# Performance work log

Hardware: AMD Instinct MI355X
Metric: run time of the kernel (lower is better)

The kernel has to match this reference:

```python
import jax, jax.numpy as jnp
import numpy as np

E, K, MULT = 8, 2, 4          # num_experts, top_k, ffn mult
CF = 1.25                     # capacity_factor


def setup_inputs() -> dict:
    key = jax.random.key(0)
    ks = jax.random.split(key, 8)
    B, T, C = 4, 2048, 1024
    H = C * MULT
    s = 0.02
    return {
        "x": jax.random.normal(ks[0], (B, T, C), jnp.float32),
        "rw": jax.random.normal(ks[1], (E, C), jnp.float32) * s,   # router weight [E,C]
        "rb": jnp.zeros((E,), jnp.float32),                        # router bias
        "w1": jax.random.normal(ks[2], (E, C, H), jnp.float32) * s,
        "b1": jnp.zeros((E, H), jnp.float32),
        "w2": jax.random.normal(ks[3], (E, H, C), jnp.float32) * s,
        "b2": jnp.zeros((E, C), jnp.float32),
    }


def reference(x, rw, rb, w1, b1, w2, b2):
    B, T, C = x.shape
    N = B * T
    cap = int(CF * N / E)                      # static capacity per expert
    xf = x.reshape(N, C)
    logits = xf @ rw.T + rb                    # [N,E]
    probs = jax.nn.softmax(logits, axis=-1)
    topk_probs, topk_idx = jax.lax.top_k(probs, K)      # [N,K]
    topk_probs = topk_probs / topk_probs.sum(-1, keepdims=True)

    # Flatten (token, choice) row-major == torch.where(mask) ordering
    flat_idx = topk_idx.reshape(-1)            # [N*K] expert id per slot
    flat_gate = topk_probs.reshape(-1)         # [N*K]
    onehot = jax.nn.one_hot(flat_idx, E, dtype=jnp.int32)          # [N*K,E]
    pos = (jnp.cumsum(onehot, axis=0) - 1)[jnp.arange(N * K), flat_idx]  # rank within expert
    keep = pos < cap                           # first-come-first-served capacity drop
    tok = jnp.arange(N * K) // K               # owning token of each slot

    # Dispatch into [E, cap] buffers; dropped slots go to a dump slot at the end
    buf = jnp.where(keep, flat_idx * cap + pos, E * cap)
    gate_buf = jnp.zeros(E * cap + 1, x.dtype).at[buf].add(flat_gate)[:E * cap]
    tok_buf = jnp.zeros(E * cap + 1, jnp.int32).at[buf].set(tok)[:E * cap]

    inp = xf[tok_buf].reshape(E, cap, C)       # gathered expert inputs
    h = jax.nn.gelu(jnp.einsum('eic,ech->eih', inp, w1) + b1[:, None, :], approximate=False)
    out = jnp.einsum('eih,ehc->eic', h, w2) + b2[:, None, :]
    out = out * gate_buf.reshape(E, cap, 1)    # empty slots have gate 0 -> zero contribution

    y = jnp.zeros((N, C), x.dtype).at[tok_buf].add(out.reshape(E * cap, C))

    # Aux load-balancing loss
    imp = probs.sum(0)
    imp = imp / imp.sum()
    load = jnp.minimum(onehot.sum(0).astype(x.dtype), cap)   # kept token counts
    load = load / load.sum()
    aux_loss = (imp * load).sum() * (E ** 2)
    return y.reshape(B, T, C), aux_loss
```

## Files before the change

kernel.cpp:

```cpp
#include <hip/hip_runtime.h>
#include <hip/hip_bf16.h>
#include <math.h>

#define NE    8
#define KTOP  2
#define CDIM  1024
#define HDIM  4096
#define NTOK  8192
#define CAPE  1280
#define NSLOT (NTOK * KTOP)
#define G1BLK 640

typedef __bf16 bf16x8 __attribute__((ext_vector_type(8)));
typedef __bf16 bf16x4 __attribute__((ext_vector_type(4)));
typedef float  f32x4  __attribute__((ext_vector_type(4)));

#define GAS __attribute__((address_space(1)))
#define LAS __attribute__((address_space(3)))

__device__ __forceinline__ void transpose64_body(
    const float* __restrict__ src, __bf16* __restrict__ dst, int R, int Cc,
    int bx, int by, int e, int t, char* sm)
{
    __bf16 (*T)[72] = (__bf16(*)[72])sm;
    const int cb = bx * 64;
    const int rb = by * 64;
    const int px = t & 15, py = t >> 4;

    const float* s = src + (size_t)e * R * Cc
                   + (size_t)(rb + py * 4) * Cc + cb + px * 4;
    float4 m[4];
#pragma unroll
    for (int i = 0; i < 4; ++i)
        m[i] = *(const float4*)(s + (size_t)i * Cc);
#pragma unroll
    for (int j = 0; j < 4; ++j) {
        bf16x4 v;
        v[0] = (__bf16)((&m[0].x)[j]);
        v[1] = (__bf16)((&m[1].x)[j]);
        v[2] = (__bf16)((&m[2].x)[j]);
        v[3] = (__bf16)((&m[3].x)[j]);
        *(bf16x4*)&T[px * 4 + j][py * 4] = v;
    }
    __syncthreads();
    const int oc = t >> 2, rc = (t & 3) * 16;
    __bf16* d = dst + (size_t)e * R * Cc + (size_t)(cb + oc) * R + rb + rc;
    *(bf16x8*)d       = *(const bf16x8*)&T[oc][rc];
    *(bf16x8*)(d + 8) = *(const bf16x8*)&T[oc][rc + 8];
}

__global__ __launch_bounds__(256) void k_prolog(
    const float* __restrict__ w1, const float* __restrict__ x,
    const float* __restrict__ rw, const float* __restrict__ rb,
    __bf16* __restrict__ w1t, float* __restrict__ probs,
    float* __restrict__ gates, int* __restrict__ tidx)
{
    __shared__ char sm[32768];
    const int bid = blockIdx.x;
    const int t   = threadIdx.x;

    if (bid < 8192) {
        const int bx = bid & 63, by = (bid >> 6) & 15, e = bid >> 10;
        transpose64_body(w1, w1t, CDIM, HDIM, bx, by, e, t, sm);
        return;
    }

    float* rws = (float*)sm;
    for (int i = t; i < NE * CDIM / 4; i += 256)
        ((float4*)rws)[i] = ((const float4*)rw)[i];
    __syncthreads();

    const int wave = t >> 6, lane = t & 63;
    const int n = (bid - 8192) * 4 + wave;
    const float* xr = x + (size_t)n * CDIM;

    float acc[NE];
#pragma unroll
    for (int e = 0; e < NE; ++e) acc[e] = 0.f;
    for (int j = 0; j < CDIM / 64; ++j) {
        const float xv = xr[j * 64 + lane];
#pragma unroll
        for (int e = 0; e < NE; ++e) acc[e] += xv * rws[e * CDIM + j * 64 + lane];
    }
#pragma unroll
    for (int off = 32; off > 0; off >>= 1) {
#pragma unroll
        for (int e = 0; e < NE; ++e) acc[e] += __shfl_down(acc[e], off);
    }
    if (lane == 0) {
        float mx = -1e30f;
#pragma unroll
        for (int e = 0; e < NE; ++e) { acc[e] += rb[e]; mx = fmaxf(mx, acc[e]); }
        float p[NE], s = 0.f;
#pragma unroll
        for (int e = 0; e < NE; ++e) { p[e] = expf(acc[e] - mx); s += p[e]; }
        const float inv = 1.f / s;
#pragma unroll
        for (int e = 0; e < NE; ++e) { p[e] *= inv; probs[(size_t)n * NE + e] = p[e]; }
        int   i1 = 0;  float v1 = p[0];
        int   i2 = -1; float v2 = -1.f;
#pragma unroll
        for (int e = 1; e < NE; ++e) {
            if (p[e] > v1)      { v2 = v1; i2 = i1; v1 = p[e]; i1 = e; }
            else if (p[e] > v2) { v2 = p[e]; i2 = e; }
        }
        const float gs = 1.f / (v1 + v2);
        gates[n * 2 + 0] = v1 * gs;  gates[n * 2 + 1] = v2 * gs;
        tidx[n * 2 + 0]  = i1;       tidx[n * 2 + 1]  = i2;
    }
}

__global__ __launch_bounds__(256) void k_scan(
    const int* __restrict__ tidx, const float* __restrict__ probs,
    int* __restrict__ slot, int* __restrict__ tok, float* __restrict__ d_aux)
{
    __shared__ int   lcnt[256][NE];
    __shared__ float ps[256][NE];
    const int t = threadIdx.x;

    for (int i = t; i < NE * CAPE; i += 256) tok[i] = 0;

    int c8[NE];
#pragma unroll
    for (int e = 0; e < NE; ++e) c8[e] = 0;
    const int per  = NSLOT / 256;
    const int base = t * per;
    for (int s = 0; s < per; ++s) c8[tidx[base + s]]++;
#pragma unroll
    for (int e = 0; e < NE; ++e) lcnt[t][e] = c8[e];

    float f8[NE];
#pragma unroll
    for (int e = 0; e < NE; ++e) f8[e] = 0.f;
    for (int n = t; n < NTOK; n += 256) {
        const float4 a = *(const float4*)(probs + (size_t)n * NE);
        const float4 b = *(const float4*)(probs + (size_t)n * NE + 4);
        f8[0] += a.x; f8[1] += a.y; f8[2] += a.z; f8[3] += a.w;
        f8[4] += b.x; f8[5] += b.y; f8[6] += b.z; f8[7] += b.w;
    }
#pragma unroll
    for (int e = 0; e < NE; ++e) ps[t][e] = f8[e];

    __syncthreads();

    int run[NE];
#pragma unroll
    for (int e = 0; e < NE; ++e) run[e] = c8[e];
    for (int d = 1; d < 256; d <<= 1) {
        int add[NE];
#pragma unroll
        for (int e = 0; e < NE; ++e) add[e] = (t >= d) ? lcnt[t - d][e] : 0;
        __syncthreads();
#pragma unroll
        for (int e = 0; e < NE; ++e) { run[e] += add[e]; lcnt[t][e] = run[e]; }
        __syncthreads();
    }
    int pre[NE], tot[NE];
#pragma unroll
    for (int e = 0; e < NE; ++e) {
        pre[e] = run[e] - c8[e];
        tot[e] = lcnt[255][e];
    }

    for (int d = 128; d >= 1; d >>= 1) {
        if (t < d) {
#pragma unroll
            for (int e = 0; e < NE; ++e) ps[t][e] += ps[t + d][e];
        }
        __syncthreads();
    }

    for (int s = 0; s < per; ++s) {
        const int sg = base + s;
        const int e  = tidx[sg];
        const int p  = pre[e]++;
        if (p < CAPE) { slot[sg] = e * CAPE + p; tok[e * CAPE + p] = sg >> 1; }
        else          { slot[sg] = -1; }
    }
    if (t == 0) {
        float isum = 0.f, lsum = 0.f, ld[NE];
#pragma unroll
        for (int e = 0; e < NE; ++e) isum += ps[0][e];
#pragma unroll
        for (int e = 0; e < NE; ++e) { ld[e] = fminf((float)tot[e], (float)CAPE); lsum += ld[e]; }
        float aux = 0.f;
#pragma unroll
        for (int e = 0; e < NE; ++e) aux += (ps[0][e] / isum) * (ld[e] / lsum);
        *d_aux = aux * (float)(NE * NE);
    }
}

__global__ __launch_bounds__(256) void k_gather(
    const float* __restrict__ x, const int* __restrict__ tok,
    __bf16* __restrict__ inp)
{
    const int row = blockIdx.x;
    const int t   = threadIdx.x;
    const int tk  = tok[row];
    const float4 v = ((const float4*)(x + (size_t)tk * CDIM))[t];
    bf16x4 o;
    o[0] = (__bf16)v.x; o[1] = (__bf16)v.y; o[2] = (__bf16)v.z; o[3] = (__bf16)v.w;
    *(bf16x4*)(inp + (size_t)row * CDIM + t * 4) = o;
}

#define MFMA_BF16 __builtin_amdgcn_mfma_f32_16x16x32_bf16
#define DSR_I(dst, addr, IMM) \
    asm volatile("ds_read_b128 %0, %1 offset:" #IMM : "=v"(dst) : "v"(addr))
#define DSR(dst, addr, IMM) DSR_I(dst, addr, IMM)
#define WVM4() asm volatile("s_waitcnt vmcnt(4)" ::: "memory")
#define SB0()  __builtin_amdgcn_sched_barrier(0)

#define PH(RDB, OA0, OA1, MB, VA0, VA1, VB0, VB1, STG, VMW)                   \
    {                                                                         \
        if (RDB) {                                                            \
            DSR(fb[0][0], VB0, 0);    DSR(fb[0][1], VB1, 0);                  \
            DSR(fb[1][0], VB0, 2048); DSR(fb[1][1], VB1, 2048);               \
            DSR(fb[2][0], VB0, 4096); DSR(fb[2][1], VB1, 4096);               \
            DSR(fb[3][0], VB0, 6144); DSR(fb[3][1], VB1, 6144);               \
        }                                                                     \
        DSR(fa[0][0], VA0, OA0); DSR(fa[0][1], VA1, OA0);                     \
        DSR(fa[1][0], VA0, OA1); DSR(fa[1][1], VA1, OA1);                     \
        STG;                                                                  \
        if (RDB) { asm volatile("s_waitcnt lgkmcnt(8)" ::: "memory"); }       \
        __builtin_amdgcn_s_barrier();                                         \
        asm volatile("s_waitcnt lgkmcnt(0)" ::: "memory");                    \
        SB0();                                                                \
        __builtin_amdgcn_s_setprio(1);                                        \
        _Pragma("unroll")                                                     \
        for (int n = 0; n < 4; ++n) {                                         \
            acc[MB][n]   = MFMA_BF16(fb[n][0], fa[0][0], acc[MB][n], 0,0,0);  \
            acc[MB][n]   = MFMA_BF16(fb[n][1], fa[0][1], acc[MB][n], 0,0,0);  \
            acc[MB+1][n] = MFMA_BF16(fb[n][0], fa[1][0], acc[MB+1][n],0,0,0); \
            acc[MB+1][n] = MFMA_BF16(fb[n][1], fa[1][1], acc[MB+1][n],0,0,0); \
        }                                                                     \
        __builtin_amdgcn_s_setprio(0);                                        \
        VMW;                                                                  \
        __builtin_amdgcn_s_barrier();                                        \
        SB0();                                                                \
    }

#define GEMM_BODY(GELU_F)                                                     \
    const int NK  = Ktot >> 6;                                                \
    const int NI  = NK >> 1;                                                  \
    const int bm  = sid / NBN, bn = sid % NBN;                                \
    const int e   = bm / mtPerE;                                              \
    const size_t row0 = (size_t)bm * 256;                                     \
    const int    col0 = bn * 256;                                             \
    const int tid = threadIdx.x;                                              \
    const int w   = tid >> 6, l = tid & 63;                                   \
    const int wr  = w >> 2, wc = w & 3;                                       \
    const int lr  = l & 15, hi = l >> 4;                                      \
    const int srow = tid >> 3;                                                \
    const int kf   = ((tid & 7) ^ (srow & 7)) << 3;                           \
    const __bf16* pA = Aall + (row0 + srow) * (size_t)Ktot + kf;              \
    const __bf16* pB = Ball + ((size_t)e * Ntot + col0 + srow) * (size_t)Ktot + kf; \
    const unsigned L0 = (unsigned)(size_t)(LAS char*)lds;                     \
    const unsigned sA00 = L0 +          w * 1024;                             \
    const unsigned sA01 = sA00 + 16384;                                       \
    const unsigned sA10 = sA00 + 32768;                                       \
    const unsigned sA11 = sA00 + 49152;                                       \
    const unsigned sB00 = sA00 + 65536;                                       \
    const unsigned sB01 = sB00 + 16384;                                       \
    const unsigned sB10 = sB00 + 32768;                                       \
    const unsigned sB11 = sB00 + 49152;                                       \
    auto SH_A = [&](unsigned dbase, int half, int kt) {                       \
        const __bf16* g = pA + (size_t)(half * 128) * Ktot + (size_t)kt * 64; \
        _Pragma("unroll")                                                     \
        for (int gg = 0; gg < 2; ++gg)                                        \
            __builtin_amdgcn_global_load_lds(                                 \
                (const GAS void*)(g + (size_t)gg * 64 * Ktot),                \
                (LAS void*)(size_t)(dbase + gg * 8192), 16, 0, 0);            \
    };                                                                        \
    auto SH_B = [&](unsigned dbase, int half, int kt) {                       \
        const __bf16* g = pB + (size_t)(half * 128) * Ktot + (size_t)kt * 64; \
        _Pragma("unroll")                                                     \
        for (int gg = 0; gg < 2; ++gg)                                        \
            __builtin_amdgcn_global_load_lds(                                 \
                (const GAS void*)(g + (size_t)gg * 64 * Ktot),                \
                (LAS void*)(size_t)(dbase + gg * 8192), 16, 0, 0);            \
    };                                                                        \
    const unsigned swz = (l & 7) << 4;                                        \
    const unsigned kb0 = ((unsigned)(hi << 4)) ^ swz;                         \
    const unsigned kb1 = ((unsigned)(64 + (hi << 4))) ^ swz;                  \
    const unsigned vA00 = L0 + (unsigned)(wr * 16384 + lr * 128) + kb0;       \
    const unsigned vA01 = L0 + (unsigned)(wr * 16384 + lr * 128) + kb1;       \
    const unsigned vA10 = vA00 + 32768, vA11 = vA01 + 32768;                  \
    const unsigned vBb  = L0 + 65536                                          \
        + (unsigned)((wc >> 1) * 16384 + ((wc & 1) * 64 + lr) * 128);         \
    const unsigned vB00 = vBb + kb0, vB01 = vBb + kb1;                        \
    const unsigned vB10 = vB00 + 32768, vB11 = vB01 + 32768;                  \
    SH_B(sB00, 0, 0); SH_B(sB01, 1, 0);                                       \
    SH_A(sA00, 0, 0); SH_A(sA01, 1, 0);                                       \
    SH_B(sB10, 0, 1); SH_B(sB11, 1, 1);                                       \
    WVM4();                                                                   \
    __builtin_amdgcn_s_barrier();                                             \
    SB0();                                                                    \
    f32x4 acc[8][4] = {};                                                     \
    bf16x8 fa[2][2], fb[4][2];                                                \
    for (int i = 0; i < NI; ++i) {                                            \
        const int t1 = 2 * i + 1;                                             \
        const int t2 = (2 * i + 2 < NK) ? 2 * i + 2 : NK - 1;                 \
        const int t3 = (2 * i + 3 < NK) ? 2 * i + 3 : NK - 1;                 \
        PH(1, 0,     2048,  0, vA00, vA01, vB00, vB01, SH_A(sA10, 0, t1), (void)0) \
        PH(0, 4096,  6144,  2, vA00, vA01, vB00, vB01, SH_A(sA11, 1, t1), (void)0) \
        PH(0, 8192,  10240, 4, vA00, vA01, vB00, vB01, SH_B(sB00, 0, t2), (void)0) \
        PH(0, 12288, 14336, 6, vA00, vA01, vB00, vB01, SH_B(sB01, 1, t2), WVM4())  \
        PH(1, 0,     2048,  0, vA10, vA11, vB10, vB11, SH_A(sA00, 0, t2), (void)0) \
        PH(0, 4096,  6144,  2, vA10, vA11, vB10, vB11, SH_A(sA01, 1, t2), (void)0) \
        PH(0, 8192,  10240, 4, vA10, vA11, vB10, vB11, SH_B(sB10, 0, t3), (void)0) \
        PH(0, 12288, 14336, 6, vA10, vA11, vB10, vB11, SH_B(sB11, 1, t3), WVM4())  \
    }                                                                         \
    asm volatile("s_waitcnt vmcnt(0)" ::: "memory");                          \
    __builtin_amdgcn_s_barrier();                                             \
    SB0();                                                                    \
    const int lrow0 = wr * 128;                                               \
    const int lcol0 = wc * 64;                                                \
    _Pragma("unroll")                                                         \
    for (int n = 0; n < 4; ++n) {                                             \
        float bbv[4] = {0.f, 0.f, 0.f, 0.f};                                  \
        if (GELU_F) {                                                         \
            const float4 b4 = *(const float4*)(biasAll + (size_t)e * Ntot     \
                                               + col0 + lcol0 + n * 16 + hi * 4); \
            bbv[0] = b4.x; bbv[1] = b4.y; bbv[2] = b4.z; bbv[3] = b4.w;       \
        }                                                                     \
        _Pragma("unroll")                                                     \
        for (int m = 0; m < 8; ++m) {                                         \
            const f32x4 v = acc[m][n];                                        \
            bf16x4 o;                                                         \
            _Pragma("unroll")                                                 \
            for (int i = 0; i < 4; ++i) {                                     \
                float t = v[i];                                               \
                if (GELU_F) {                                                 \
                    t += bbv[i];                                              \
                    const float u  = 0.7978845608028654f * (t + 0.044715f * t * t * t); \
                    const float ex = __expf(2.f * u);                         \
                    t = t * (1.f - 1.f / (ex + 1.f));                         \
                }                                                             \
                o[i] = (__bf16)t;                                             \
            }                                                                 \
            *(bf16x4*)(lds + (lrow0 + m * 16 + lr) * 520                      \
                           + (lcol0 + n * 16 + hi * 4) * 2) = o;              \
        }                                                                     \
    }                                                                         \
    __builtin_amdgcn_s_barrier();                                             \
    {                                                                         \
        const int rr0 = tid >> 5;                                             \
        const int cc  = (tid & 31) * 8;                                       \
        _Pragma("unroll")                                                     \
        for (int it = 0; it < 16; ++it) {                                     \
            const int rr = it * 16 + rr0;                                     \
            const bf16x8 v = *(const bf16x8*)(lds + rr * 520 + cc * 2);       \
            *(bf16x8*)(Call + (row0 + rr) * (size_t)Ntot + col0 + cc) = v;    \
        }                                                                     \
    }

__global__ __launch_bounds__(512, 2) void k_g1w2t(
    const __bf16* __restrict__ Aall, const __bf16* __restrict__ Ball,
    const float* __restrict__ biasAll, __bf16* __restrict__ Call,
    const float* __restrict__ w2, __bf16* __restrict__ w2t)
{
    __shared__ char lds[133120];

    if (blockIdx.x < G1BLK) {
        const int Ktot = CDIM, Ntot = HDIM, NBN = HDIM / 256, mtPerE = CAPE / 256;
        const int id  = blockIdx.x;
        const int sid = (id & 7) * (G1BLK >> 3) + (id >> 3);
        GEMM_BODY(true)
        return;
    }

    const int b2   = blockIdx.x - G1BLK;
    const int sub  = threadIdx.x >> 8;
    const int t    = threadIdx.x & 255;
    const int tile = b2 * 2 + sub;
    const int bx = tile & 15, by = (tile >> 4) & 63, e = tile >> 10;
    transpose64_body(w2, w2t, HDIM, CDIM, bx, by, e, t, lds + sub * 9216);
}

__global__ __launch_bounds__(512, 2) void k_gemm8(
    const __bf16* __restrict__ Aall, const __bf16* __restrict__ Ball,
    const float* __restrict__ biasAll, __bf16* __restrict__ Call,
    int Ktot, int Ntot, int NBN, int mtPerE)
{
    __shared__ char lds[133120];
    const int cpx = gridDim.x >> 3;
    const int id  = blockIdx.x;
    const int sid = (id & 7) * cpx + (id >> 3);
    GEMM_BODY(false)
}

__global__ __launch_bounds__(256) void k_combine(
    const __bf16* __restrict__ outb, const int* __restrict__ slot,
    const float* __restrict__ gates, const int* __restrict__ tidx,
    const float* __restrict__ b2, float* __restrict__ y)
{
    const int n = blockIdx.x;
    const int t = threadIdx.x;
    const int c = t * 4;
    float r0 = 0.f, r1 = 0.f, r2 = 0.f, r3 = 0.f;
#pragma unroll
    for (int k = 0; k < KTOP; ++k) {
        const int s = slot[n * 2 + k];
        if (s < 0) continue;
        const float g = gates[n * 2 + k];
        const int   e = tidx[n * 2 + k];
        const bf16x4 v = *(const bf16x4*)(outb + (size_t)s * CDIM + c);
        const float4 bb = *(const float4*)(b2 + (size_t)e * CDIM + c);
        r0 += g * ((float)v[0] + bb.x);
        r1 += g * ((float)v[1] + bb.y);
        r2 += g * ((float)v[2] + bb.z);
        r3 += g * ((float)v[3] + bb.w);
    }
    float4 o = make_float4(r0, r1, r2, r3);
    *(float4*)(y + (size_t)n * CDIM + c) = o;
}

extern "C" void kernel_launch(void* const* d_in, const int* in_sizes, int n_in,
                              void* d_out, int out_size, void* d_ws, size_t ws_size,
                              hipStream_t stream)
{
    const float* x  = (const float*)d_in[0];
    const float* rw = (const float*)d_in[1];
    const float* rb = (const float*)d_in[2];
    const float* w1 = (const float*)d_in[3];
    const float* b1 = (const float*)d_in[4];
    const float* w2 = (const float*)d_in[5];
    const float* b2 = (const float*)d_in[6];
    float* y = (float*)d_out;

    char* ws = (char*)d_ws;
    size_t off = 0;
    auto alloc = [&](size_t bytes) -> void* {
        void* p = ws + off;
        off = (off + bytes + 255) & ~(size_t)255;
        return p;
    };
    __bf16* w1t  = (__bf16*)alloc((size_t)NE * CDIM * HDIM * 2);
    __bf16* w2t  = (__bf16*)alloc((size_t)NE * CDIM * HDIM * 2);
    __bf16* inp  = (__bf16*)alloc((size_t)NE * CAPE * CDIM * 2);
    __bf16* hbuf = (__bf16*)alloc((size_t)NE * CAPE * HDIM * 2);
    __bf16* outb = (__bf16*)alloc((size_t)NE * CAPE * CDIM * 2);
    float*  probs = (float*)alloc((size_t)NTOK * NE * 4);
    float*  gates = (float*)alloc((size_t)NTOK * 2 * 4);
    int*    tidx  = (int*)alloc((size_t)NTOK * 2 * 4);
    int*    slot  = (int*)alloc((size_t)NTOK * 2 * 4);
    int*    tok   = (int*)alloc((size_t)NE * CAPE * 4);

    k_prolog<<<8192 + NTOK / 4, 256, 0, stream>>>(
        w1, x, rw, rb, w1t, probs, gates, tidx);

    k_scan<<<1, 256, 0, stream>>>(tidx, probs, slot, tok, y + (size_t)NTOK * CDIM);

    k_gather<<<NE * CAPE, 256, 0, stream>>>(x, tok, inp);

    k_g1w2t<<<G1BLK + 4096, 512, 0, stream>>>(inp, w1t, b1, hbuf, w2, w2t);

    k_gemm8<<<dim3((NE * CAPE / 256) * (CDIM / 256)), 512, 0, stream>>>(
        hbuf, w2t, nullptr, outb, HDIM, CDIM, CDIM / 256, CAPE / 256);

    k_combine<<<NTOK, 256, 0, stream>>>(outb, slot, gates, tidx, b2, y);
}
```

Before: 354.7 us.

## Restructure GEMM k-tile inner loop into 4x2 quadrant MFMA phases

Replaces the eight per-phase blocks, each doing LDS reads for two A rows and all four B columns with two barriers, with a k-tile schedule of four quadrant phases. Each phase loads four A fragments and two B fragments and issues 16 MFMAs before a single barrier. This is meant to raise MFMA work per barrier and per LDS read and to cut barrier count, so LDS traffic and global staging overlap better. It doubles the A fragment registers, which may hurt occupancy, and it changes where the staging stores sit relative to the barriers, so LDS race safety depends on the new ordering.

Result: no change. 353.5 us (-0.3%).

```diff
diff --git a/kernel.cpp b/kernel.cpp
--- a/kernel.cpp
+++ b/kernel.cpp
@@ -208,35 +208,57 @@
     asm volatile("ds_read_b128 %0, %1 offset:" #IMM : "=v"(dst) : "v"(addr))
 #define DSR(dst, addr, IMM) DSR_I(dst, addr, IMM)
 #define WVM4() asm volatile("s_waitcnt vmcnt(4)" ::: "memory")
+#define WLG0() asm volatile("s_waitcnt lgkmcnt(0)" ::: "memory")
 #define SB0()  __builtin_amdgcn_sched_barrier(0)
 
-#define PH(RDB, OA0, OA1, MB, VA0, VA1, VB0, VB1, STG, VMW)                   \
-    {                                                                         \
-        if (RDB) {                                                            \
-            DSR(fb[0][0], VB0, 0);    DSR(fb[0][1], VB1, 0);                  \
-            DSR(fb[1][0], VB0, 2048); DSR(fb[1][1], VB1, 2048);               \
-            DSR(fb[2][0], VB0, 4096); DSR(fb[2][1], VB1, 4096);               \
-            DSR(fb[3][0], VB0, 6144); DSR(fb[3][1], VB1, 6144);               \
-        }                                                                     \
-        DSR(fa[0][0], VA0, OA0); DSR(fa[0][1], VA1, OA0);                     \
-        DSR(fa[1][0], VA0, OA1); DSR(fa[1][1], VA1, OA1);                     \
-        STG;                                                                  \
-        if (RDB) { asm volatile("s_waitcnt lgkmcnt(8)" ::: "memory"); }       \
-        __builtin_amdgcn_s_barrier();                                         \
-        asm volatile("s_waitcnt lgkmcnt(0)" ::: "memory");                    \
-        SB0();                                                                \
-        __builtin_amdgcn_s_setprio(1);                                        \
-        _Pragma("unroll")                                                     \
-        for (int n = 0; n < 4; ++n) {                                         \
-            acc[MB][n]   = MFMA_BF16(fb[n][0], fa[0][0], acc[MB][n], 0,0,0);  \
-            acc[MB][n]   = MFMA_BF16(fb[n][1], fa[0][1], acc[MB][n], 0,0,0);  \
-            acc[MB+1][n] = MFMA_BF16(fb[n][0], fa[1][0], acc[MB+1][n],0,0,0); \
-            acc[MB+1][n] = MFMA_BF16(fb[n][1], fa[1][1], acc[MB+1][n],0,0,0); \
-        }                                                                     \
-        __builtin_amdgcn_s_setprio(0);                                        \
-        VMW;                                                                  \
-        __builtin_amdgcn_s_barrier();                                        \
-        SB0();                                                                \
+#define QMFMA(MROW, NB)                                                      \
+    __builtin_amdgcn_s_setprio(1);                                           \
+    _Pragma("unroll")                                                        \
+    for (int n = 0; n < 2; ++n) {                                            \
+        _Pragma("unroll")                                                    \
+        for (int m = 0; m < 4; ++m) {                                        \
+            acc[(MROW) + m][(NB) + n] = MFMA_BF16(fb[(NB) + n][0], fa[m][0], \
+                acc[(MROW) + m][(NB) + n], 0, 0, 0);                         \
+            acc[(MROW) + m][(NB) + n] = MFMA_BF16(fb[(NB) + n][1], fa[m][1], \
+                acc[(MROW) + m][(NB) + n], 0, 0, 0);                         \
+        }                                                                    \
+    }                                                                        \
+    __builtin_amdgcn_s_setprio(0);
+
+#define KTILE(VA0, VA1, VB0, VB1, STG1, STG2, STG3, STG4)                    \
+    {                                                                        \
+                                          \
+        DSR(fa[0][0], VA0, 0);    DSR(fa[0][1], VA1, 0);                     \
+        DSR(fa[1][0], VA0, 2048); DSR(fa[1][1], VA1, 2048);                  \
+        DSR(fa[2][0], VA0, 4096); DSR(fa[2][1], VA1, 4096);                  \
+        DSR(fa[3][0], VA0, 6144); DSR(fa[3][1], VA1, 6144);                  \
+        DSR(fb[0][0], VB0, 0);    DSR(fb[0][1], VB1, 0);                     \
+        DSR(fb[1][0], VB0, 2048); DSR(fb[1][1], VB1, 2048);                  \
+        STG1;                                                                \
+        WLG0(); SB0();                                                       \
+        QMFMA(0, 0)                                                          \
+        __builtin_amdgcn_s_barrier(); SB0();                                 \
+                                                        \
+        DSR(fb[2][0], VB0, 4096); DSR(fb[2][1], VB1, 4096);                  \
+        DSR(fb[3][0], VB0, 6144); DSR(fb[3][1], VB1, 6144);                  \
+        STG2;                                                                \
+        WLG0(); SB0();                                                       \
+        QMFMA(0, 2)                                                          \
+        __builtin_amdgcn_s_barrier(); SB0();                                 \
+                                                        \
+        DSR(fa[0][0], VA0, 8192);  DSR(fa[0][1], VA1, 8192);                 \
+        DSR(fa[1][0], VA0, 10240); DSR(fa[1][1], VA1, 10240);                \
+        DSR(fa[2][0], VA0, 12288); DSR(fa[2][1], VA1, 12288);                \
+        DSR(fa[3][0], VA0, 14336); DSR(fa[3][1], VA1, 14336);                \
+        STG3;                                                                \
+        WLG0(); SB0();                                                       \
+        QMFMA(4, 0)                                                          \
+        __builtin_amdgcn_s_barrier(); SB0();                                 \
+                                                           \
+        STG4;                                                                \
+        QMFMA(4, 2)                                                          \
+        WVM4();                                                              \
+        __builtin_amdgcn_s_barrier(); SB0();                                 \
     }
 
 #define GEMM_BODY(GELU_F)                                                     \
@@ -296,19 +318,17 @@
     __builtin_amdgcn_s_barrier();                                             \
     SB0();                                                                    \
     f32x4 acc[8][4] = {};                                                     \
-    bf16x8 fa[2][2], fb[4][2];                                                \
+    bf16x8 fa[4][2], fb[4][2];                                                \
     for (int i = 0; i < NI; ++i) {                                            \
         const int t1 = 2 * i + 1;                                             \
         const int t2 = (2 * i + 2 < NK) ? 2 * i + 2 : NK - 1;                 \
         const int t3 = (2 * i + 3 < NK) ? 2 * i + 3 : NK - 1;                 \
-        PH(1, 0,     2048,  0, vA00, vA01, vB00, vB01, SH_A(sA10, 0, t1), (void)0) \
-        PH(0, 4096,  6144,  2, vA00, vA01, vB00, vB01, SH_A(sA11, 1, t1), (void)0) \
-        PH(0, 8192,  10240, 4, vA00, vA01, vB00, vB01, SH_B(sB00, 0, t2), (void)0) \
-        PH(0, 12288, 14336, 6, vA00, vA01, vB00, vB01, SH_B(sB01, 1, t2), WVM4())  \
-        PH(1, 0,     2048,  0, vA10, vA11, vB10, vB11, SH_A(sA00, 0, t2), (void)0) \
-        PH(0, 4096,  6144,  2, vA10, vA11, vB10, vB11, SH_A(sA01, 1, t2), (void)0) \
-        PH(0, 8192,  10240, 4, vA10, vA11, vB10, vB11, SH_B(sB10, 0, t3), (void)0) \
-        PH(0, 12288, 14336, 6, vA10, vA11, vB10, vB11, SH_B(sB11, 1, t3), WVM4())  \
+        KTILE(vA00, vA01, vB00, vB01,                                         \
+              SH_A(sA10, 0, t1), SH_A(sA11, 1, t1),                           \
+              SH_B(sB00, 0, t2), SH_B(sB01, 1, t2))                           \
+        KTILE(vA10, vA11, vB10, vB11,                                         \
+              SH_A(sA00, 0, t2), SH_A(sA01, 1, t2),                           \
+              SH_B(sB10, 0, t3), SH_B(sB11, 1, t3))                           \
     }                                                                         \
     asm volatile("s_waitcnt vmcnt(0)" ::: "memory");                          \
     __builtin_amdgcn_s_barrier();                                             \
```
